# Kernel tuning notes

Hardware: AMD Instinct MI355X
Metric: run time of the kernel (lower is better)

## Reference

```python
import jax, jax.numpy as jnp
import numpy as np

B, T, D = 4, 2048, 1024
H, DK = 8, 64
EPS = 1e-6

def _xavier(key, shape):
    fan_in, fan_out = shape[1], shape[0]
    lim = float(np.sqrt(6.0 / (fan_in + fan_out)))
    return jax.random.uniform(key, shape, jnp.float32, -lim, lim)

def setup_inputs() -> dict:
    key = jax.random.key(0)
    ks = jax.random.split(key, 7)
    x = jax.random.normal(ks[0], (B, T, D), jnp.float32)
    W_Q = _xavier(ks[1], (H * DK, D))
    W_K = _xavier(ks[2], (H * DK, D))
    W_V = _xavier(ks[3], (H * DK, D))
    W_g_w = _xavier(ks[4], (H * DK, D))
    W_g_b = jax.random.normal(ks[5], (H * DK,), jnp.float32) * 0.02
    W_O = _xavier(ks[6], (D, H * DK))
    decay_log = jnp.zeros((H,), jnp.float32)
    return {"x": x, "W_Q": W_Q, "W_K": W_K, "W_V": W_V,
            "W_g_w": W_g_w, "W_g_b": W_g_b, "W_O": W_O,
            "decay_log": decay_log}

def _phi(u):
    # ELU + 1 feature map (positive)
    return jax.nn.elu(u) + 1.0

def reference(x, W_Q, W_K, W_V, W_g_w, W_g_b, W_O, decay_log):
    b, t, d = x.shape
    q = _phi((x @ W_Q.T).reshape(b, t, H, DK))
    k = _phi((x @ W_K.T).reshape(b, t, H, DK))
    v = (x @ W_V.T).reshape(b, t, H, DK)
    gamma = jax.nn.sigmoid(decay_log)           # [H]
    g4 = gamma[None, :, None, None]             # [1,H,1,1]
    g3 = gamma[None, :, None]                   # [1,H,1]

    # time-major for scan: [T,B,H,DK]
    qT = jnp.moveaxis(q, 1, 0)
    kT = jnp.moveaxis(k, 1, 0)
    vT = jnp.moveaxis(v, 1, 0)

    S0 = jnp.zeros((b, H, DK, DK), x.dtype)
    z0 = jnp.zeros((b, H, DK), x.dtype)

    def step(carry, inp):
        S, z = carry
        qt, kt, vt = inp
        S = g4 * S + jnp.einsum('bhi,bhj->bhij', kt, vt)
        z = g3 * z + kt
        num = jnp.einsum('bhij,bhi->bhj', S, qt)
        den = jnp.sum(z * qt, axis=-1, keepdims=True) + EPS
        return (S, z), num / den

    _, ys = jax.lax.scan(step, (S0, z0), (qT, kT, vT))  # ys: [T,B,H,DK]
    outputs = jnp.moveaxis(ys, 0, 1)                    # [B,T,H,DK]

    gate = jax.nn.sigmoid(x @ W_g_w.T + W_g_b).reshape(b, t, H, DK)
    y = (outputs * gate).reshape(b, t, H * DK)
    return y @ W_O.T
```

## Files before the change

### kernel.cpp

```cpp
#include <hip/hip_runtime.h>
#include <cstdint>
#include <cstddef>

#define B_   4
#define T_   2048
#define D_   1024
#define H_   8
#define DK_  64
#define HD_  512
#define CH_  64
#define NC_  32
#define EPS_ 1e-6f

typedef __attribute__((ext_vector_type(4))) float f32x4;
typedef __attribute__((ext_vector_type(8))) short s16x8;

__device__ __forceinline__ unsigned short f2bf(float f) {
    unsigned int x = __float_as_uint(f);
    unsigned int r = (x + 0x7FFFu + ((x >> 16) & 1u)) >> 16;
    return (unsigned short)r;
}
__device__ __forceinline__ float bf2f(unsigned short u) {
    return __uint_as_float(((unsigned int)u) << 16);
}
__device__ __forceinline__ void ld4(const float* p, float* o) {
    float4 v = *(const float4*)p; o[0]=v.x; o[1]=v.y; o[2]=v.z; o[3]=v.w;
}
__device__ __forceinline__ void gl_lds16(const unsigned short* g, unsigned short* l) {
    __builtin_amdgcn_global_load_lds(
        (const __attribute__((address_space(1))) unsigned int*)g,
        (__attribute__((address_space(3))) unsigned int*)l, 16, 0, 0);
}

__global__ __launch_bounds__(256) void k_cvt_all(
    const float* __restrict__ x,
    const float* __restrict__ wq, const float* __restrict__ wk,
    const float* __restrict__ wv, const float* __restrict__ wgw,
    const float* __restrict__ wo,
    unsigned short* __restrict__ xb,
    unsigned short* __restrict__ wqb, unsigned short* __restrict__ wkb,
    unsigned short* __restrict__ wvb, unsigned short* __restrict__ wgb,
    unsigned short* __restrict__ wob)
{
    int bid = blockIdx.x;
    const float* src; unsigned short* dst; int idx;
    if (bid < 8192) {
        src = x; dst = xb; idx = bid * 256 + threadIdx.x;
    } else {
        int r = bid - 8192;
        int w = r >> 9;
        idx = (r & 511) * 256 + threadIdx.x;
        switch (w) {
            case 0:  src = wq;  dst = wqb; break;
            case 1:  src = wk;  dst = wkb; break;
            case 2:  src = wv;  dst = wvb; break;
            case 3:  src = wgw; dst = wgb; break;
            default: src = wo;  dst = wob; break;
        }
    }
    float4 v = ((const float4*)src)[idx];
    ushort4 o;
    o.x = f2bf(v.x); o.y = f2bf(v.y); o.z = f2bf(v.z); o.w = f2bf(v.w);
    ((ushort4*)dst)[idx] = o;
}

#define GT_M 128
#define GT_N 128
#define GBK  64
#define LDA  64

__global__ __launch_bounds__(256) void k_gemm_qkvg(
    const unsigned short* __restrict__ xb,
    const unsigned short* __restrict__ wqb, const unsigned short* __restrict__ wkb,
    const unsigned short* __restrict__ wvb, const unsigned short* __restrict__ wgb,
    const float* __restrict__ bias,
    unsigned short* __restrict__ qo, unsigned short* __restrict__ ko,
    unsigned short* __restrict__ vo, unsigned short* __restrict__ go)
{
    __shared__ unsigned short As[GT_M * LDA];
    __shared__ unsigned short Bs[GT_N * LDA];
    const int tid = threadIdx.x;
    const int id  = blockIdx.x;
    const int xcd = id & 7, per = id >> 3;
    const int mtile = xcd * 8 + (per & 7);
    const int combo = per >> 3;
    const int which = combo >> 2;
    const int nb    = combo & 3;
    const int m0    = mtile * GT_M;
    const int n0    = nb * GT_N;
    const unsigned short* Wp = (which == 0) ? wqb : (which == 1) ? wkb : (which == 2) ? wvb : wgb;
    unsigned short* Op       = (which == 0) ? qo  : (which == 1) ? ko  : (which == 2) ? vo  : go;
    const int K = D_;

    const int lane = tid & 63, wave = tid >> 6;
    const int wm = (wave >> 1) * 64, wn = (wave & 1) * 64;
    const int r16 = lane & 15, quad = lane >> 4;
    const int lrow = lane >> 3, lseg = lane & 7;
    const int sseg = lseg ^ lrow;
    const int rx   = r16 & 7;

    f32x4 acc[4][4];
    #pragma unroll
    for (int a = 0; a < 4; a++)
        #pragma unroll
        for (int b = 0; b < 4; b++) acc[a][b] = 0.0f;

    for (int ko_ = 0; ko_ < K; ko_ += GBK) {
        #pragma unroll
        for (int i = 0; i < 4; i++) {
            int chunk = wave * 4 + i;
            int row = chunk * 8 + lrow;
            gl_lds16(xb + (size_t)(m0 + row) * K + ko_ + sseg * 8, As + chunk * 512);
            gl_lds16(Wp + (size_t)(n0 + row) * K + ko_ + sseg * 8, Bs + chunk * 512);
        }
        __syncthreads();
        #pragma unroll
        for (int kk = 0; kk < GBK; kk += 32) {
            const int gb_ = kk >> 3;
            const int goff = (((gb_ + quad) ^ rx) << 3);
            s16x8 af[4], bf[4];
            #pragma unroll
            for (int mt = 0; mt < 4; mt++)
                af[mt] = *(const s16x8*)&As[(wm + mt * 16 + r16) * LDA + goff];
            #pragma unroll
            for (int nt = 0; nt < 4; nt++)
                bf[nt] = *(const s16x8*)&Bs[(wn + nt * 16 + r16) * LDA + goff];
            #pragma unroll
            for (int mt = 0; mt < 4; mt++)
                #pragma unroll
                for (int nt = 0; nt < 4; nt++)
                    acc[mt][nt] = __builtin_amdgcn_mfma_f32_16x16x32_bf16(af[mt], bf[nt], acc[mt][nt], 0, 0, 0);
        }
        __syncthreads();
    }
    #pragma unroll
    for (int mt = 0; mt < 4; mt++) {
        #pragma unroll
        for (int nt = 0; nt < 4; nt++) {
            int col = n0 + wn + nt * 16 + r16;
            float bv = (which == 3) ? bias[col] : 0.0f;
            #pragma unroll
            for (int r = 0; r < 4; r++) {
                int row = m0 + wm + mt * 16 + quad * 4 + r;
                float v = acc[mt][nt][r];
                if (which <= 1)      v = (v > 0.0f) ? v + 1.0f : __builtin_expf(v);
                else if (which == 3) v = 1.0f / (1.0f + __builtin_expf(-(v + bv)));
                Op[(size_t)row * HD_ + col] = f2bf(v);
            }
        }
    }
}

__global__ __launch_bounds__(256) void k_gemm_out(
    const unsigned short* __restrict__ ogb, const unsigned short* __restrict__ wob,
    float* __restrict__ y)
{
    __shared__ unsigned short As[GT_M * LDA];
    __shared__ unsigned short Bs[GT_N * LDA];
    const int tid = threadIdx.x;
    const int id  = blockIdx.x;
    const int xcd = id & 7, per = id >> 3;
    const int m0 = (xcd * 8 + (per & 7)) * GT_M;
    const int n0 = (per >> 3) * GT_N;
    const int K = HD_;

    const int lane = tid & 63, wave = tid >> 6;
    const int wm = (wave >> 1) * 64, wn = (wave & 1) * 64;
    const int r16 = lane & 15, quad = lane >> 4;
    const int lrow = lane >> 3, lseg = lane & 7;
    const int sseg = lseg ^ lrow;
    const int rx   = r16 & 7;

    f32x4 acc[4][4];
    #pragma unroll
    for (int a = 0; a < 4; a++)
        #pragma unroll
        for (int b = 0; b < 4; b++) acc[a][b] = 0.0f;

    for (int ko_ = 0; ko_ < K; ko_ += GBK) {
        #pragma unroll
        for (int i = 0; i < 4; i++) {
            int chunk = wave * 4 + i;
            int row = chunk * 8 + lrow;
            gl_lds16(ogb + (size_t)(m0 + row) * K + ko_ + sseg * 8, As + chunk * 512);
            gl_lds16(wob + (size_t)(n0 + row) * K + ko_ + sseg * 8, Bs + chunk * 512);
        }
        __syncthreads();
        #pragma unroll
        for (int kk = 0; kk < GBK; kk += 32) {
            const int gb_ = kk >> 3;
            const int goff = (((gb_ + quad) ^ rx) << 3);
            s16x8 af[4], bf[4];
            #pragma unroll
            for (int mt = 0; mt < 4; mt++)
                af[mt] = *(const s16x8*)&As[(wm + mt * 16 + r16) * LDA + goff];
            #pragma unroll
            for (int nt = 0; nt < 4; nt++)
                bf[nt] = *(const s16x8*)&Bs[(wn + nt * 16 + r16) * LDA + goff];
            #pragma unroll
            for (int mt = 0; mt < 4; mt++)
                #pragma unroll
                for (int nt = 0; nt < 4; nt++)
                    acc[mt][nt] = __builtin_amdgcn_mfma_f32_16x16x32_bf16(af[mt], bf[nt], acc[mt][nt], 0, 0, 0);
        }
        __syncthreads();
    }
    #pragma unroll
    for (int mt = 0; mt < 4; mt++)
        #pragma unroll
        for (int nt = 0; nt < 4; nt++) {
            int col = n0 + wn + nt * 16 + r16;
            #pragma unroll
            for (int r = 0; r < 4; r++) {
                int row = m0 + wm + mt * 16 + quad * 4 + r;
                y[(size_t)row * D_ + col] = acc[mt][nt][r];
            }
        }
}

__global__ __launch_bounds__(256) void k_chunk_sums(
    const unsigned short* __restrict__ Kb, const unsigned short* __restrict__ Vb,
    float* __restrict__ Ssum, float* __restrict__ zsum, const float* __restrict__ decay_log)
{
    __shared__ float kl[CH_ * 68];
    __shared__ float vl[CH_ * 68];
    const int tid = threadIdx.x;
    const int bc  = blockIdx.x;
    const int c   = bc & (NC_ - 1);
    const int bh  = bc >> 5;
    const int h   = bh & (H_ - 1);
    const int b   = bh >> 3;
    const float g  = 1.0f / (1.0f + __builtin_expf(-decay_log[h]));
    const float lg = __builtin_log2f(g);
    const int t0 = c * CH_;

    #pragma unroll
    for (int e = 0; e < 2; e++) {
        int lid = e * 256 + tid;
        int l = lid >> 3, d0 = (lid & 7) * 8;
        float w = __builtin_exp2f((float)(CH_ - 1 - l) * lg);
        size_t gidx = (size_t)(b * T_ + t0 + l) * HD_ + h * DK_ + d0;
        uint4 kraw = *(const uint4*)(Kb + gidx);
        uint4 vraw = *(const uint4*)(Vb + gidx);
        const unsigned short* kp = (const unsigned short*)&kraw;
        const unsigned short* vp = (const unsigned short*)&vraw;
        #pragma unroll
        for (int j = 0; j < 8; j++) {
            kl[l * 68 + d0 + j] = bf2f(kp[j]) * w;
            vl[l * 68 + d0 + j] = bf2f(vp[j]);
        }
    }
    __syncthreads();

    const int ti = tid >> 4, tj = tid & 15;
    const int i0 = ti * 4, j0 = tj * 4;
    float acc[4][4];
    #pragma unroll
    for (int r = 0; r < 4; r++)
        #pragma unroll
        for (int cc = 0; cc < 4; cc++) acc[r][cc] = 0.0f;

    for (int l = 0; l < CH_; l++) {
        float kv[4], vv[4];
        ld4(&kl[l * 68 + i0], kv);
        ld4(&vl[l * 68 + j0], vv);
        #pragma unroll
        for (int r = 0; r < 4; r++)
            #pragma unroll
            for (int cc = 0; cc < 4; cc++) acc[r][cc] += kv[r] * vv[cc];
    }
    size_t base = (size_t)bc * (DK_ * DK_);
    #pragma unroll
    for (int r = 0; r < 4; r++) {
        float4 st = make_float4(acc[r][0], acc[r][1], acc[r][2], acc[r][3]);
        *(float4*)&Ssum[base + (size_t)(i0 + r) * DK_ + j0] = st;
    }
    if (tid < DK_) {
        float s = 0.0f;
        for (int l = 0; l < CH_; l++) s += kl[l * 68 + tid];
        zsum[(size_t)bc * DK_ + tid] = s;
    }
}

__global__ __launch_bounds__(256) void k_chunk_out(
    const unsigned short* __restrict__ Qb, const unsigned short* __restrict__ Kb,
    const unsigned short* __restrict__ Vb, const unsigned short* __restrict__ Gb,
    const float* __restrict__ Ssum, const float* __restrict__ zsum,
    unsigned short* __restrict__ OGb, const float* __restrict__ decay_log)
{
    __shared__ float BufA[CH_ * 68];
    __shared__ float BufB[CH_ * 68];
    __shared__ float BufC[CH_ * 68];
    __shared__ float den_l[CH_];
    __shared__ float zp_l[DK_];
    __shared__ float gpow[CH_ + 1];

    const int tid = threadIdx.x;
    const int bc  = blockIdx.x;
    const int c   = bc & (NC_ - 1);
    const int bh  = bc >> 5;
    const int h   = bh & (H_ - 1);
    const int b   = bh >> 3;
    const float g  = 1.0f / (1.0f + __builtin_expf(-decay_log[h]));
    const float lg = __builtin_log2f(g);
    const float gC = __builtin_exp2f((float)CH_ * lg);
    const int t0 = c * CH_;

    if (tid <= CH_) gpow[tid] = __builtin_exp2f((float)tid * lg);

    {
        f32x4 sp[4];
        #pragma unroll
        for (int q = 0; q < 4; q++) sp[q] = 0.0f;
        const int flat = tid * 16;
        for (int cp = 0; cp < c; cp++) {
            const float* src = Ssum + (size_t)(bh * NC_ + cp) * 4096 + flat;
            #pragma unroll
            for (int q = 0; q < 4; q++) {
                f32x4 v = *(const f32x4*)(src + q * 4);
                sp[q] = sp[q] * gC + v;
            }
        }
        int row = tid >> 2, col0 = (tid & 3) * 16;
        #pragma unroll
        for (int q = 0; q < 4; q++)
            *(f32x4*)&BufC[row * 68 + col0 + q * 4] = sp[q];
    }
    if (tid < DK_) {
        float zp = 0.0f;
        for (int cp = 0; cp < c; cp++)
            zp = zp * gC + zsum[(size_t)(bh * NC_ + cp) * DK_ + tid];
        zp_l[tid] = zp;
    }

    #pragma unroll
    for (int e = 0; e < 2; e++) {
        int lid = e * 256 + tid;
        int l = lid >> 3, d0 = (lid & 7) * 8;
        size_t gidx = (size_t)(b * T_ + t0 + l) * HD_ + h * DK_ + d0;
        uint4 qraw = *(const uint4*)(Qb + gidx);
        uint4 kraw = *(const uint4*)(Kb + gidx);
        const unsigned short* qp = (const unsigned short*)&qraw;
        const unsigned short* kp = (const unsigned short*)&kraw;
        #pragma unroll
        for (int j = 0; j < 8; j++) {
            BufA[(d0 + j) * 68 + l] = bf2f(qp[j]);
            BufB[(d0 + j) * 68 + l] = bf2f(kp[j]);
        }
    }
    __syncthreads();

    const int ti = tid >> 4, tj = tid & 15;
    const int i0 = ti * 4, j0 = tj * 4;
    float sc[4][4], it[4][4];
    #pragma unroll
    for (int r = 0; r < 4; r++)
        #pragma unroll
        for (int cc = 0; cc < 4; cc++) { sc[r][cc] = 0.0f; it[r][cc] = 0.0f; }

    for (int d = 0; d < DK_; d++) {
        float qv[4], kv[4], sv[4];
        ld4(&BufA[d * 68 + i0], qv);
        ld4(&BufB[d * 68 + j0], kv);
        ld4(&BufC[d * 68 + j0], sv);
        #pragma unroll
        for (int r = 0; r < 4; r++)
            #pragma unroll
            for (int cc = 0; cc < 4; cc++) {
                sc[r][cc] += qv[r] * kv[cc];
                it[r][cc] += qv[r] * sv[cc];
            }
    }
    #pragma unroll
    for (int r = 0; r < 4; r++) {
        int i = i0 + r;
        #pragma unroll
        for (int cc = 0; cc < 4; cc++) {
            int jl = j0 + cc;
            sc[r][cc] = (jl <= i) ? sc[r][cc] * gpow[i - jl] : 0.0f;
            it[r][cc] *= gpow[i + 1];
        }
        float rs = sc[r][0] + sc[r][1] + sc[r][2] + sc[r][3];
        rs += __shfl_xor(rs, 1);
        rs += __shfl_xor(rs, 2);
        rs += __shfl_xor(rs, 4);
        rs += __shfl_xor(rs, 8);
        if (tj == 0) den_l[i] = rs;
    }
    __syncthreads();
    if (tid < DK_) {
        float dp = 0.0f;
        for (int d = 0; d < DK_; d++) dp += BufA[d * 68 + tid] * zp_l[d];
        den_l[tid] += gpow[tid + 1] * dp + EPS_;
    }
    __syncthreads();
    #pragma unroll
    for (int cc = 0; cc < 4; cc++) {
        float4 st = make_float4(sc[0][cc], sc[1][cc], sc[2][cc], sc[3][cc]);
        *(float4*)&BufA[(j0 + cc) * 68 + i0] = st;
    }
    #pragma unroll
    for (int e = 0; e < 2; e++) {
        int lid = e * 256 + tid;
        int l = lid >> 3, d0 = (lid & 7) * 8;
        size_t gidx = (size_t)(b * T_ + t0 + l) * HD_ + h * DK_ + d0;
        uint4 vraw = *(const uint4*)(Vb + gidx);
        const unsigned short* vp = (const unsigned short*)&vraw;
        #pragma unroll
        for (int j = 0; j < 8; j++) BufB[l * 68 + d0 + j] = bf2f(vp[j]);
    }
    __syncthreads();

    float og[4][4];
    #pragma unroll
    for (int r = 0; r < 4; r++)
        #pragma unroll
        for (int cc = 0; cc < 4; cc++) og[r][cc] = it[r][cc];

    for (int jl = 0; jl < CH_; jl++) {
        float scv[4], vv[4];
        ld4(&BufA[jl * 68 + i0], scv);
        ld4(&BufB[jl * 68 + j0], vv);
        #pragma unroll
        for (int r = 0; r < 4; r++)
            #pragma unroll
            for (int cc = 0; cc < 4; cc++) og[r][cc] += scv[r] * vv[cc];
    }
    #pragma unroll
    for (int r = 0; r < 4; r++) {
        int i = i0 + r;
        float rcp = 1.0f / den_l[i];
        size_t gidx = (size_t)(b * T_ + t0 + i) * HD_ + h * DK_ + j0;
        ushort4 graw = *(const ushort4*)(Gb + gidx);
        ushort4 o;
        o.x = f2bf(og[r][0] * rcp * bf2f(graw.x));
        o.y = f2bf(og[r][1] * rcp * bf2f(graw.y));
        o.z = f2bf(og[r][2] * rcp * bf2f(graw.z));
        o.w = f2bf(og[r][3] * rcp * bf2f(graw.w));
        *(ushort4*)(OGb + gidx) = o;
    }
}

extern "C" void kernel_launch(void* const* d_in, const int* in_sizes, int n_in,
                              void* d_out, int out_size, void* d_ws, size_t ws_size,
                              hipStream_t stream)
{
    (void)in_sizes; (void)n_in; (void)out_size; (void)ws_size;
    const float* x         = (const float*)d_in[0];
    const float* W_Q       = (const float*)d_in[1];
    const float* W_K       = (const float*)d_in[2];
    const float* W_V       = (const float*)d_in[3];
    const float* W_gw      = (const float*)d_in[4];
    const float* W_gb      = (const float*)d_in[5];
    const float* W_O       = (const float*)d_in[6];
    const float* decay_log = (const float*)d_in[7];
    float* y = (float*)d_out;

    char* ws = (char*)d_ws;
    size_t off = 0;
    auto alloc = [&](size_t bytes) { void* p = ws + off; off += (bytes + 255) & ~(size_t)255; return p; };
    unsigned short* xb   = (unsigned short*)alloc((size_t)B_ * T_ * D_ * 2);
    unsigned short* wqb  = (unsigned short*)alloc((size_t)HD_ * D_ * 2);
    unsigned short* wkb  = (unsigned short*)alloc((size_t)HD_ * D_ * 2);
    unsigned short* wvb  = (unsigned short*)alloc((size_t)HD_ * D_ * 2);
    unsigned short* wgb  = (unsigned short*)alloc((size_t)HD_ * D_ * 2);
    unsigned short* wob  = (unsigned short*)alloc((size_t)D_ * HD_ * 2);
    unsigned short* qb   = (unsigned short*)alloc((size_t)B_ * T_ * HD_ * 2);
    unsigned short* kb   = (unsigned short*)alloc((size_t)B_ * T_ * HD_ * 2);
    unsigned short* vb   = (unsigned short*)alloc((size_t)B_ * T_ * HD_ * 2);
    unsigned short* gb   = (unsigned short*)alloc((size_t)B_ * T_ * HD_ * 2);
    unsigned short* ogb  = (unsigned short*)alloc((size_t)B_ * T_ * HD_ * 2);
    float* Ssum = (float*)alloc((size_t)B_ * H_ * NC_ * DK_ * DK_ * 4);
    float* zsum = (float*)alloc((size_t)B_ * H_ * NC_ * DK_ * 4);

    k_cvt_all<<<8192 + 5 * 512, 256, 0, stream>>>(x, W_Q, W_K, W_V, W_gw, W_O,
                                                  xb, wqb, wkb, wvb, wgb, wob);
    k_gemm_qkvg<<<1024, 256, 0, stream>>>(xb, wqb, wkb, wvb, wgb, W_gb, qb, kb, vb, gb);
    k_chunk_sums<<<B_ * H_ * NC_, 256, 0, stream>>>(kb, vb, Ssum, zsum, decay_log);
    k_chunk_out<<<B_ * H_ * NC_, 256, 0, stream>>>(qb, kb, vb, gb, Ssum, zsum, ogb, decay_log);
    k_gemm_out<<<512, 256, 0, stream>>>(ogb, wob, y);
}
```

Baseline: 242.9 us.

## Use bf16 MFMA for chunk state sums and intra-chunk attention matmuls

Replaces the scalar FP32 outer-product loops in the chunk-sum and chunk-output kernels with 16x16x32 bf16 MFMA instructions. Shared-memory tiles are stored as bf16 in transposed layouts padded to stride 72, and V is loaded together with Q/K up front. The aim is to move the per-chunk matmul work onto the matrix cores and halve LDS footprint. In exchange, the decayed K, the prefix state and the masked score matrix are rounded to bf16, which adds error to the recurrence output.

```diff
diff --git a/kernel.cpp b/kernel.cpp
--- a/kernel.cpp
+++ b/kernel.cpp
@@ -22,9 +22,6 @@
 }
 __device__ __forceinline__ float bf2f(unsigned short u) {
     return __uint_as_float(((unsigned int)u) << 16);
-}
-__device__ __forceinline__ void ld4(const float* p, float* o) {
-    float4 v = *(const float4*)p; o[0]=v.x; o[1]=v.y; o[2]=v.z; o[3]=v.w;
 }
 __device__ __forceinline__ void gl_lds16(const unsigned short* g, unsigned short* l) {
     __builtin_amdgcn_global_load_lds(
@@ -218,12 +215,14 @@
         }
 }
 
+#define LDB 72
+
 __global__ __launch_bounds__(256) void k_chunk_sums(
     const unsigned short* __restrict__ Kb, const unsigned short* __restrict__ Vb,
     float* __restrict__ Ssum, float* __restrict__ zsum, const float* __restrict__ decay_log)
 {
-    __shared__ float kl[CH_ * 68];
-    __shared__ float vl[CH_ * 68];
+    __shared__ unsigned short kT[CH_ * LDB];
+    __shared__ unsigned short vT[CH_ * LDB];
     const int tid = threadIdx.x;
     const int bc  = blockIdx.x;
     const int c   = bc & (NC_ - 1);
@@ -246,38 +245,38 @@
         const unsigned short* vp = (const unsigned short*)&vraw;
         #pragma unroll
         for (int j = 0; j < 8; j++) {
-            kl[l * 68 + d0 + j] = bf2f(kp[j]) * w;
-            vl[l * 68 + d0 + j] = bf2f(vp[j]);
+            kT[(d0 + j) * LDB + l] = f2bf(bf2f(kp[j]) * w);
+            vT[(d0 + j) * LDB + l] = vp[j];
         }
     }
     __syncthreads();
 
-    const int ti = tid >> 4, tj = tid & 15;
-    const int i0 = ti * 4, j0 = tj * 4;
-    float acc[4][4];
-    #pragma unroll
-    for (int r = 0; r < 4; r++)
-        #pragma unroll
-        for (int cc = 0; cc < 4; cc++) acc[r][cc] = 0.0f;
-
-    for (int l = 0; l < CH_; l++) {
-        float kv[4], vv[4];
-        ld4(&kl[l * 68 + i0], kv);
-        ld4(&vl[l * 68 + j0], vv);
+    const int lane = tid & 63, wave = tid >> 6;
+    const int r16 = lane & 15, quad = lane >> 4;
+    const int wm = wave * 16;
+
+    f32x4 acc[4];
+    #pragma unroll
+    for (int nt = 0; nt < 4; nt++) acc[nt] = 0.0f;
+    #pragma unroll
+    for (int ls_ = 0; ls_ < CH_; ls_ += 32) {
+        s16x8 a = *(const s16x8*)&kT[(wm + r16) * LDB + ls_ + quad * 8];
+        #pragma unroll
+        for (int nt = 0; nt < 4; nt++) {
+            s16x8 bv = *(const s16x8*)&vT[(nt * 16 + r16) * LDB + ls_ + quad * 8];
+            acc[nt] = __builtin_amdgcn_mfma_f32_16x16x32_bf16(a, bv, acc[nt], 0, 0, 0);
+        }
+    }
+    size_t base = (size_t)bc * (DK_ * DK_);
+    #pragma unroll
+    for (int nt = 0; nt < 4; nt++)
         #pragma unroll
         for (int r = 0; r < 4; r++)
-            #pragma unroll
-            for (int cc = 0; cc < 4; cc++) acc[r][cc] += kv[r] * vv[cc];
-    }
-    size_t base = (size_t)bc * (DK_ * DK_);
-    #pragma unroll
-    for (int r = 0; r < 4; r++) {
-        float4 st = make_float4(acc[r][0], acc[r][1], acc[r][2], acc[r][3]);
-        *(float4*)&Ssum[base + (size_t)(i0 + r) * DK_ + j0] = st;
-    }
+            Ssum[base + (size_t)(wm + quad * 4 + r) * DK_ + nt * 16 + r16] = acc[nt][r];
+
     if (tid < DK_) {
         float s = 0.0f;
-        for (int l = 0; l < CH_; l++) s += kl[l * 68 + tid];
+        for (int l = 0; l < CH_; l++) s += bf2f(kT[tid * LDB + l]);
         zsum[(size_t)bc * DK_ + tid] = s;
     }
 }
@@ -288,9 +287,10 @@
     const float* __restrict__ Ssum, const float* __restrict__ zsum,
     unsigned short* __restrict__ OGb, const float* __restrict__ decay_log)
 {
-    __shared__ float BufA[CH_ * 68];
-    __shared__ float BufB[CH_ * 68];
-    __shared__ float BufC[CH_ * 68];
+    __shared__ unsigned short qs[CH_ * LDB];
+    __shared__ unsigned short ks_l[CH_ * LDB];
+    __shared__ unsigned short SpT[CH_ * LDB];
+    __shared__ unsigned short vT[CH_ * LDB];
     __shared__ float den_l[CH_];
     __shared__ float zp_l[DK_];
     __shared__ float gpow[CH_ + 1];
@@ -308,31 +308,6 @@
 
     if (tid <= CH_) gpow[tid] = __builtin_exp2f((float)tid * lg);
 
-    {
-        f32x4 sp[4];
-        #pragma unroll
-        for (int q = 0; q < 4; q++) sp[q] = 0.0f;
-        const int flat = tid * 16;
-        for (int cp = 0; cp < c; cp++) {
-            const float* src = Ssum + (size_t)(bh * NC_ + cp) * 4096 + flat;
-            #pragma unroll
-            for (int q = 0; q < 4; q++) {
-                f32x4 v = *(const f32x4*)(src + q * 4);
-                sp[q] = sp[q] * gC + v;
-            }
-        }
-        int row = tid >> 2, col0 = (tid & 3) * 16;
-        #pragma unroll
-        for (int q = 0; q < 4; q++)
-            *(f32x4*)&BufC[row * 68 + col0 + q * 4] = sp[q];
-    }
-    if (tid < DK_) {
-        float zp = 0.0f;
-        for (int cp = 0; cp < c; cp++)
-            zp = zp * gC + zsum[(size_t)(bh * NC_ + cp) * DK_ + tid];
-        zp_l[tid] = zp;
-    }
-
     #pragma unroll
     for (int e = 0; e < 2; e++) {
         int lid = e * 256 + tid;
@@ -340,104 +315,112 @@
         size_t gidx = (size_t)(b * T_ + t0 + l) * HD_ + h * DK_ + d0;
         uint4 qraw = *(const uint4*)(Qb + gidx);
         uint4 kraw = *(const uint4*)(Kb + gidx);
-        const unsigned short* qp = (const unsigned short*)&qraw;
-        const unsigned short* kp = (const unsigned short*)&kraw;
-        #pragma unroll
-        for (int j = 0; j < 8; j++) {
-            BufA[(d0 + j) * 68 + l] = bf2f(qp[j]);
-            BufB[(d0 + j) * 68 + l] = bf2f(kp[j]);
-        }
+        uint4 vraw = *(const uint4*)(Vb + gidx);
+        *(uint4*)&qs[l * LDB + d0]   = qraw;
+        *(uint4*)&ks_l[l * LDB + d0] = kraw;
+        const unsigned short* vp = (const unsigned short*)&vraw;
+        #pragma unroll
+        for (int j = 0; j < 8; j++) vT[(d0 + j) * LDB + l] = vp[j];
+    }
+    {
+        f32x4 sp[4];
+        #pragma unroll
+        for (int q = 0; q < 4; q++) sp[q] = 0.0f;
+        const int flat = tid * 16;
+        for (int cp = 0; cp < c; cp++) {
+            const float* src = Ssum + (size_t)(bh * NC_ + cp) * 4096 + flat;
+            #pragma unroll
+            for (int q = 0; q < 4; q++) {
+                f32x4 v = *(const f32x4*)(src + q * 4);
+                sp[q] = sp[q] * gC + v;
+            }
+        }
+        int row = tid >> 2, col0 = (tid & 3) * 16;
+        #pragma unroll
+        for (int q = 0; q < 4; q++)
+            #pragma unroll
+            for (int e = 0; e < 4; e++)
+                SpT[(col0 + q * 4 + e) * LDB + row] = f2bf(sp[q][e]);
+    }
+    if (tid < DK_) {
+        float zp = 0.0f;
+        for (int cp = 0; cp < c; cp++)
+            zp = zp * gC + zsum[(size_t)(bh * NC_ + cp) * DK_ + tid];
+        zp_l[tid] = zp;
     }
     __syncthreads();
 
-    const int ti = tid >> 4, tj = tid & 15;
-    const int i0 = ti * 4, j0 = tj * 4;
-    float sc[4][4], it[4][4];
-    #pragma unroll
-    for (int r = 0; r < 4; r++)
-        #pragma unroll
-        for (int cc = 0; cc < 4; cc++) { sc[r][cc] = 0.0f; it[r][cc] = 0.0f; }
-
-    for (int d = 0; d < DK_; d++) {
-        float qv[4], kv[4], sv[4];
-        ld4(&BufA[d * 68 + i0], qv);
-        ld4(&BufB[d * 68 + j0], kv);
-        ld4(&BufC[d * 68 + j0], sv);
-        #pragma unroll
-        for (int r = 0; r < 4; r++)
-            #pragma unroll
-            for (int cc = 0; cc < 4; cc++) {
-                sc[r][cc] += qv[r] * kv[cc];
-                it[r][cc] += qv[r] * sv[cc];
-            }
+    const int lane = tid & 63, wave = tid >> 6;
+    const int r16 = lane & 15, quad = lane >> 4;
+    const int wm = wave * 16;
+
+    f32x4 P[4], IT[4];
+    #pragma unroll
+    for (int nt = 0; nt < 4; nt++) { P[nt] = 0.0f; IT[nt] = 0.0f; }
+    #pragma unroll
+    for (int ks_ = 0; ks_ < DK_; ks_ += 32) {
+        s16x8 a = *(const s16x8*)&qs[(wm + r16) * LDB + ks_ + quad * 8];
+        #pragma unroll
+        for (int nt = 0; nt < 4; nt++) {
+            s16x8 bk = *(const s16x8*)&ks_l[(nt * 16 + r16) * LDB + ks_ + quad * 8];
+            P[nt] = __builtin_amdgcn_mfma_f32_16x16x32_bf16(a, bk, P[nt], 0, 0, 0);
+            s16x8 bs = *(const s16x8*)&SpT[(nt * 16 + r16) * LDB + ks_ + quad * 8];
+            IT[nt] = __builtin_amdgcn_mfma_f32_16x16x32_bf16(a, bs, IT[nt], 0, 0, 0);
+        }
+    }
+    __syncthreads();
+
+    float rowsum[4] = {0.f, 0.f, 0.f, 0.f};
+    #pragma unroll
+    for (int nt = 0; nt < 4; nt++) {
+        #pragma unroll
+        for (int r = 0; r < 4; r++) {
+            int i = wm + quad * 4 + r, j = nt * 16 + r16;
+            float s = (j <= i) ? P[nt][r] * gpow[i - j] : 0.0f;
+            rowsum[r] += s;
+            SpT[i * LDB + j] = f2bf(s);
+            IT[nt][r] *= gpow[i + 1];
+        }
     }
     #pragma unroll
     for (int r = 0; r < 4; r++) {
-        int i = i0 + r;
-        #pragma unroll
-        for (int cc = 0; cc < 4; cc++) {
-            int jl = j0 + cc;
-            sc[r][cc] = (jl <= i) ? sc[r][cc] * gpow[i - jl] : 0.0f;
-            it[r][cc] *= gpow[i + 1];
-        }
-        float rs = sc[r][0] + sc[r][1] + sc[r][2] + sc[r][3];
+        float rs = rowsum[r];
         rs += __shfl_xor(rs, 1);
         rs += __shfl_xor(rs, 2);
         rs += __shfl_xor(rs, 4);
         rs += __shfl_xor(rs, 8);
-        if (tj == 0) den_l[i] = rs;
+        if (r16 == 0) den_l[wm + quad * 4 + r] = rs;
     }
     __syncthreads();
+
     if (tid < DK_) {
         float dp = 0.0f;
-        for (int d = 0; d < DK_; d++) dp += BufA[d * 68 + tid] * zp_l[d];
+        for (int d = 0; d < DK_; d++) dp += bf2f(qs[tid * LDB + d]) * zp_l[d];
         den_l[tid] += gpow[tid + 1] * dp + EPS_;
     }
+    f32x4 O[4];
+    #pragma unroll
+    for (int nt = 0; nt < 4; nt++) O[nt] = IT[nt];
+    #pragma unroll
+    for (int ls_ = 0; ls_ < CH_; ls_ += 32) {
+        s16x8 a = *(const s16x8*)&SpT[(wm + r16) * LDB + ls_ + quad * 8];
+        #pragma unroll
+        for (int nt = 0; nt < 4; nt++) {
+            s16x8 bv = *(const s16x8*)&vT[(nt * 16 + r16) * LDB + ls_ + quad * 8];
+            O[nt] = __builtin_amdgcn_mfma_f32_16x16x32_bf16(a, bv, O[nt], 0, 0, 0);
+        }
+    }
     __syncthreads();
-    #pragma unroll
-    for (int cc = 0; cc < 4; cc++) {
-        float4 st = make_float4(sc[0][cc], sc[1][cc], sc[2][cc], sc[3][cc]);
-        *(float4*)&BufA[(j0 + cc) * 68 + i0] = st;
-    }
-    #pragma unroll
-    for (int e = 0; e < 2; e++) {
-        int lid = e * 256 + tid;
-        int l = lid >> 3, d0 = (lid & 7) * 8;
-        size_t gidx = (size_t)(b * T_ + t0 + l) * HD_ + h * DK_ + d0;
-        uint4 vraw = *(const uint4*)(Vb + gidx);
-        const unsigned short* vp = (const unsigned short*)&vraw;
-        #pragma unroll
-        for (int j = 0; j < 8; j++) BufB[l * 68 + d0 + j] = bf2f(vp[j]);
-    }
-    __syncthreads();
-
-    float og[4][4];
-    #pragma unroll
-    for (int r = 0; r < 4; r++)
-        #pragma unroll
-        for (int cc = 0; cc < 4; cc++) og[r][cc] = it[r][cc];
-
-    for (int jl = 0; jl < CH_; jl++) {
-        float scv[4], vv[4];
-        ld4(&BufA[jl * 68 + i0], scv);
-        ld4(&BufB[jl * 68 + j0], vv);
-        #pragma unroll
-        for (int r = 0; r < 4; r++)
-            #pragma unroll
-            for (int cc = 0; cc < 4; cc++) og[r][cc] += scv[r] * vv[cc];
-    }
-    #pragma unroll
-    for (int r = 0; r < 4; r++) {
-        int i = i0 + r;
-        float rcp = 1.0f / den_l[i];
-        size_t gidx = (size_t)(b * T_ + t0 + i) * HD_ + h * DK_ + j0;
-        ushort4 graw = *(const ushort4*)(Gb + gidx);
-        ushort4 o;
-        o.x = f2bf(og[r][0] * rcp * bf2f(graw.x));
-        o.y = f2bf(og[r][1] * rcp * bf2f(graw.y));
-        o.z = f2bf(og[r][2] * rcp * bf2f(graw.z));
-        o.w = f2bf(og[r][3] * rcp * bf2f(graw.w));
-        *(ushort4*)(OGb + gidx) = o;
+
+    #pragma unroll
+    for (int nt = 0; nt < 4; nt++) {
+        #pragma unroll
+        for (int r = 0; r < 4; r++) {
+            int i = wm + quad * 4 + r, j = nt * 16 + r16;
+            size_t gidx = (size_t)(b * T_ + t0 + i) * HD_ + h * DK_ + j;
+            float val = O[nt][r] / den_l[i] * bf2f(Gb[gidx]);
+            OGb[gidx] = f2bf(val);
+        }
     }
 }
 
```

Result: faster. 222.0 us (-8.6%).
